# Kernel tuning notes

Hardware: AMD Instinct MI355X
Metric: run time of the kernel (lower is better)

The kernel has to match this reference:

```python
import jax, jax.numpy as jnp
import numpy as np

B, T, INPUT_DIM = 4, 2048, 1024
N_HEADS, HEAD_DIM, EMB_DIM = 16, 64, 1024


def setup_inputs() -> dict:
    key = jax.random.key(0)
    ks = jax.random.split(key, 7)
    s = 0.02
    return {
        "k": jax.random.normal(ks[0], (B, T, INPUT_DIM), jnp.float32),
        "q": jax.random.normal(ks[1], (B, T, INPUT_DIM), jnp.float32),
        "v": jax.random.normal(ks[2], (B, T, INPUT_DIM), jnp.float32),
        # weights stored [in, out] (torch Linear applies x @ W.T with W [out,in])
        "w_key": jax.random.normal(ks[3], (INPUT_DIM, N_HEADS * HEAD_DIM), jnp.float32) * s,
        "w_query": jax.random.normal(ks[4], (INPUT_DIM, N_HEADS * HEAD_DIM), jnp.float32) * s,
        "w_value": jax.random.normal(ks[5], (INPUT_DIM, N_HEADS * HEAD_DIM), jnp.float32) * s,
        "w_proj": jax.random.normal(ks[6], (N_HEADS * HEAD_DIM, EMB_DIM), jnp.float32) * s,
    }


def reference(k, q, v, w_key, w_query, w_value, w_proj):
    temperature = np.sqrt(HEAD_DIM).astype(np.float32)
    # projections -> [B, T, H, D]
    kh = (k @ w_key).reshape(B, T, N_HEADS, HEAD_DIM)
    qh = (q @ w_query).reshape(B, T, N_HEADS, HEAD_DIM)
    vh = (v @ w_value).reshape(B, T, N_HEADS, HEAD_DIM)
    # scaled dot-product attention: scores [B, H, T, T]
    scores = jnp.einsum("bqhd,bkhd->bhqk", qh, kh) / temperature
    attn = jax.nn.softmax(scores, axis=-1)
    out = jnp.einsum("bhqk,bkhd->bqhd", attn, vh).reshape(B, T, N_HEADS * HEAD_DIM)
    return out @ w_proj
```

## Files before the change

### kernel.cpp

```cpp
#include <hip/hip_runtime.h>

typedef unsigned short bf16_t;
typedef __attribute__((ext_vector_type(8))) short short8;
typedef __attribute__((ext_vector_type(4))) float f32x4;
typedef __attribute__((ext_vector_type(16))) float f32x16;
typedef __attribute__((ext_vector_type(4))) unsigned short usx4;

#define T_SEQ 2048
#define NHEAD 16

__device__ __forceinline__ unsigned short f2bf(float x) {
  union { float f; unsigned u; } v; v.f = x;
  unsigned r = v.u + 0x7fffu + ((v.u >> 16) & 1u);
  return (unsigned short)(r >> 16);
}

__device__ __forceinline__ void gld_lds16(const void* g, void* l) {
  __builtin_amdgcn_global_load_lds((const __attribute__((address_space(1))) void*)g,
                                   (__attribute__((address_space(3))) void*)l, 16, 0, 0);
}

__device__ __forceinline__ unsigned cvtpk(float lo, float hi) {
  unsigned r;
  asm("v_cvt_pk_bf16_f32 %0, %1, %2" : "=v"(r) : "v"(lo), "v"(hi));
  return r;
}

__global__ __launch_bounds__(256) void cvt3(const float* __restrict__ a,
                                            const float* __restrict__ b,
                                            const float* __restrict__ c,
                                            bf16_t* __restrict__ oa,
                                            bf16_t* __restrict__ ob,
                                            bf16_t* __restrict__ oc, int n4seg) {
  int i = blockIdx.x * 256 + threadIdx.x;
  const int stride = gridDim.x * 256;
  const int total = 3 * n4seg;
  for (; i < total; i += stride) {
    const int seg = i / n4seg;
    const int j = i - seg * n4seg;
    const float* in = (seg == 0) ? a : (seg == 1) ? b : c;
    bf16_t* out = (seg == 0) ? oa : (seg == 1) ? ob : oc;
    const float4 v = ((const float4*)in)[j];
    usx4 w = { f2bf(v.x), f2bf(v.y), f2bf(v.z), f2bf(v.w) };
    ((usx4*)out)[j] = w;
  }
}

__global__ __launch_bounds__(256) void wtrans(const float* __restrict__ w0, const float* __restrict__ w1,
                                              const float* __restrict__ w2, const float* __restrict__ w3,
                                              bf16_t* __restrict__ wt) {
  __shared__ float tile[32][33];
  const float* w = (blockIdx.z == 0) ? w0 : (blockIdx.z == 1) ? w1 : (blockIdx.z == 2) ? w2 : w3;
  bf16_t* o = wt + (size_t)blockIdx.z * 1024 * 1024;
  const int c = threadIdx.x & 31;
  const int r = threadIdx.x >> 5;
  const int k0 = blockIdx.y * 32, n0 = blockIdx.x * 32;
#pragma unroll
  for (int rr = 0; rr < 32; rr += 8)
    tile[r + rr][c] = w[(size_t)(k0 + r + rr) * 1024 + n0 + c];
  __syncthreads();
#pragma unroll
  for (int rr = 0; rr < 32; rr += 8)
    o[(size_t)(n0 + r + rr) * 1024 + k0 + c] = f2bf(tile[c][r + rr]);
}

__global__ __launch_bounds__(256) void gemm_qkv(const bf16_t* __restrict__ A0,
                                                const bf16_t* __restrict__ A1,
                                                const bf16_t* __restrict__ A2,
                                                const bf16_t* __restrict__ Wt,
                                                bf16_t* __restrict__ C0,
                                                bf16_t* __restrict__ C1,
                                                bf16_t* __restrict__ C2) {
  __shared__ bf16_t As[2][128 * 64];
  __shared__ bf16_t Bs[2][128 * 64];
  const int K = 1024;
  const int z = blockIdx.z;
  const bf16_t* A  = (z == 0) ? A0 : (z == 1) ? A1 : A2;
  const bf16_t* Bt = Wt + (size_t)z * 1024 * 1024;
  const int tid = threadIdx.x;
  const int lane = tid & 63;
  const int l15 = lane & 15;
  const int g = lane >> 4;
  const int wave = tid >> 6;
  const int wr = wave >> 1, wc = wave & 1;
  const int f = blockIdx.x + (int)gridDim.x * blockIdx.y;
  const int fp = (f & 7) * 64 + (f >> 3);
  const int col0 = (fp & 7) * 128, row0 = (fp >> 3) * 128;

  f32x4 acc[4][4];
#pragma unroll
  for (int m = 0; m < 4; ++m)
#pragma unroll
    for (int n = 0; n < 4; ++n) acc[m][n] = (f32x4){0.f, 0.f, 0.f, 0.f};

  const int r_st = tid >> 3;
  const int c_st = tid & 7;

  auto stage = [&](int kt, int bi) {
#pragma unroll
    for (int i = 0; i < 4; ++i) {
      const int r = r_st + i * 32;
      gld_lds16(A  + (size_t)(row0 + r) * K + kt + c_st * 8, As[bi] + (size_t)(tid + i * 256) * 8);
      gld_lds16(Bt + (size_t)(col0 + r) * K + kt + c_st * 8, Bs[bi] + (size_t)(tid + i * 256) * 8);
    }
  };

  const int NIT = K / 64;
  stage(0, 0);
  stage(64, 1);

  for (int it = 0; it < NIT; ++it) {
    const int cur = it & 1;
    if (it + 1 < NIT) { asm volatile("s_waitcnt vmcnt(8)" ::: "memory"); }
    else              { asm volatile("s_waitcnt vmcnt(0)" ::: "memory"); }
    __builtin_amdgcn_s_barrier();
    __builtin_amdgcn_sched_barrier(0);
#pragma unroll
    for (int ks = 0; ks < 2; ++ks) {
      short8 a[4], b[4];
#pragma unroll
      for (int m = 0; m < 4; ++m)
        a[m] = *(const short8*)(As[cur] + (wr * 64 + m * 16 + l15) * 64 + ks * 32 + g * 8);
#pragma unroll
      for (int n = 0; n < 4; ++n)
        b[n] = *(const short8*)(Bs[cur] + (wc * 64 + n * 16 + l15) * 64 + ks * 32 + g * 8);
#pragma unroll
      for (int m = 0; m < 4; ++m)
#pragma unroll
        for (int n = 0; n < 4; ++n)
          acc[m][n] = __builtin_amdgcn_mfma_f32_16x16x32_bf16(a[m], b[n], acc[m][n], 0, 0, 0);
    }
    __builtin_amdgcn_s_barrier();
    __builtin_amdgcn_sched_barrier(0);
    if (it + 2 < NIT) stage((it + 2) * 64, cur);
  }

  if (z == 2) {
#pragma unroll
    for (int m = 0; m < 4; ++m) {
      const int row = row0 + wr * 64 + m * 16 + g * 4;
      const int bb = row >> 11;
      const int t = row & 2047;
#pragma unroll
      for (int n = 0; n < 4; ++n) {
        const int col = col0 + wc * 64 + n * 16 + l15;
        const int hh = col >> 6, dd = col & 63;
        usx4 w = { f2bf(acc[m][n][0]), f2bf(acc[m][n][1]), f2bf(acc[m][n][2]), f2bf(acc[m][n][3]) };
        *(usx4*)(C2 + (((size_t)(bb * 16 + hh) * 64 + dd) * 2048 + t)) = w;
      }
    }
  } else {
    const float sc = (z == 1) ? 0.18033688011112042f : 1.0f;
    bf16_t* C = (z == 1) ? C1 : C0;
#pragma unroll
    for (int m = 0; m < 4; ++m) {
      const int row = row0 + wr * 64 + m * 16 + g * 4;
#pragma unroll
      for (int n = 0; n < 4; ++n) {
        const int col = col0 + wc * 64 + n * 16 + l15;
#pragma unroll
        for (int i = 0; i < 4; ++i)
          C[(size_t)(row + i) * 1024 + col] = f2bf(acc[m][n][i] * sc);
      }
    }
  }
}

__global__ __launch_bounds__(256) void gemm_proj(const bf16_t* __restrict__ A,
                                                 const bf16_t* __restrict__ Bt,
                                                 float* __restrict__ C, int K) {
  __shared__ bf16_t As[2][128 * 64];
  __shared__ bf16_t Bs[2][128 * 64];
  const int tid = threadIdx.x;
  const int lane = tid & 63;
  const int l15 = lane & 15;
  const int g = lane >> 4;
  const int wave = tid >> 6;
  const int wr = wave >> 1, wc = wave & 1;
  const int f = blockIdx.x + (int)gridDim.x * blockIdx.y;
  const int fp = (f & 7) * 64 + (f >> 3);
  const int col0 = (fp & 7) * 128, row0 = (fp >> 3) * 128;

  f32x4 acc[4][4];
#pragma unroll
  for (int m = 0; m < 4; ++m)
#pragma unroll
    for (int n = 0; n < 4; ++n) acc[m][n] = (f32x4){0.f, 0.f, 0.f, 0.f};

  const int r_st = tid >> 3;
  const int c_st = tid & 7;

  auto stage = [&](int kt, int bi) {
#pragma unroll
    for (int i = 0; i < 4; ++i) {
      const int r = r_st + i * 32;
      gld_lds16(A  + (size_t)(row0 + r) * K + kt + c_st * 8, As[bi] + (size_t)(tid + i * 256) * 8);
      gld_lds16(Bt + (size_t)(col0 + r) * K + kt + c_st * 8, Bs[bi] + (size_t)(tid + i * 256) * 8);
    }
  };

  const int NIT = K / 64;
  stage(0, 0);
  stage(64, 1);

  for (int it = 0; it < NIT; ++it) {
    const int cur = it & 1;
    if (it + 1 < NIT) { asm volatile("s_waitcnt vmcnt(8)" ::: "memory"); }
    else              { asm volatile("s_waitcnt vmcnt(0)" ::: "memory"); }
    __builtin_amdgcn_s_barrier();
    __builtin_amdgcn_sched_barrier(0);
#pragma unroll
    for (int ks = 0; ks < 2; ++ks) {
      short8 a[4], b[4];
#pragma unroll
      for (int m = 0; m < 4; ++m)
        a[m] = *(const short8*)(As[cur] + (wr * 64 + m * 16 + l15) * 64 + ks * 32 + g * 8);
#pragma unroll
      for (int n = 0; n < 4; ++n)
        b[n] = *(const short8*)(Bs[cur] + (wc * 64 + n * 16 + l15) * 64 + ks * 32 + g * 8);
#pragma unroll
      for (int m = 0; m < 4; ++m)
#pragma unroll
        for (int n = 0; n < 4; ++n)
          acc[m][n] = __builtin_amdgcn_mfma_f32_16x16x32_bf16(a[m], b[n], acc[m][n], 0, 0, 0);
    }
    __builtin_amdgcn_s_barrier();
    __builtin_amdgcn_sched_barrier(0);
    if (it + 2 < NIT) stage((it + 2) * 64, cur);
  }

#pragma unroll
  for (int m = 0; m < 4; ++m) {
    const int row = row0 + wr * 64 + m * 16 + g * 4;
#pragma unroll
    for (int n = 0; n < 4; ++n) {
      const int col = col0 + wc * 64 + n * 16 + l15;
#pragma unroll
      for (int i = 0; i < 4; ++i)
        C[(size_t)(row + i) * 1024 + col] = acc[m][n][i];
    }
  }
}

__global__ __launch_bounds__(256) void attn_fwd(const bf16_t* __restrict__ qh,
                                                const bf16_t* __restrict__ kh,
                                                const bf16_t* __restrict__ vt,
                                                bf16_t* __restrict__ ao) {
  __shared__ bf16_t smem[24576];
  const int tid = threadIdx.x;
  const int lane = tid & 63;
  const int l31 = lane & 31;
  const int half = lane >> 5;
  const int wave = tid >> 6;
  const int f = blockIdx.x + (int)gridDim.x * blockIdx.y;
  const int fp = (f & 7) * 128 + (f >> 3);
  const int qblk = fp & 15;
  const int bh = fp >> 4;
  const int b = bh >> 4, h = bh & 15;

  const int tq = qblk * 128 + wave * 32 + l31;
  const size_t qoff = (size_t)(b * T_SEQ + tq) * 1024 + h * 64;
  short8 qf[4];
#pragma unroll
  for (int ks = 0; ks < 4; ++ks)
    qf[ks] = *(const short8*)(qh + qoff + ks * 16 + half * 8);

  union { short8 v; unsigned u[4]; } onesf;
#pragma unroll
  for (int i = 0; i < 4; ++i) onesf.u[i] = 0x3F803F80u;

  f32x16 ov0, ov1, lacc, zv;
#pragma unroll
  for (int i = 0; i < 16; ++i) { ov0[i] = 0.f; ov1[i] = 0.f; lacc[i] = 0.f; zv[i] = 0.f; }

  int off[2][4];
#pragma unroll
  for (int k = 0; k < 4; ++k) {
    const int swz = ((k * 2 + half) ^ (l31 & 7)) * 8;
    off[0][k] = l31 * 64 + swz;
    off[1][k] = (32 + l31) * 64 + swz;
  }

  const size_t kbase = (size_t)b * T_SEQ * 1024 + h * 64;
  const size_t vbase = (size_t)bh * 64 * T_SEQ;
  const int r_st = tid >> 3;
  const int cd = tid & 7;

  bf16_t* p0 = smem;
  bf16_t* p1 = smem + 8192;
  bf16_t* p2 = smem + 16384;

  auto stage = [&](int kvt, bf16_t* buf) {
    const int t0 = kvt * 64;
#pragma unroll
    for (int i = 0; i < 2; ++i) {
      const int r = r_st + i * 32;
      const int cs = cd ^ (r & 7);
      gld_lds16(kh + kbase + (size_t)(t0 + r) * 1024 + cs * 8, buf + (size_t)(tid + i * 256) * 8);
      gld_lds16(vt + vbase + (size_t)r * T_SEQ + t0 + cs * 8,  buf + 4096 + (size_t)(tid + i * 256) * 8);
    }
  };

  const int NT = T_SEQ / 64;
  stage(0, p0);
  stage(1, p1);
  asm volatile("s_waitcnt vmcnt(0)" ::: "memory");

  for (int kv = 0; kv < NT; ++kv) {
    if (kv + 1 < NT) { asm volatile("s_waitcnt vmcnt(4)" ::: "memory"); }
    else             { asm volatile("s_waitcnt vmcnt(0)" ::: "memory"); }
    __builtin_amdgcn_s_barrier();
    __builtin_amdgcn_sched_barrier(0);
    if (kv + 2 < NT) stage(kv + 2, p2);

    const bf16_t* Ks = p0;
    const bf16_t* Vs = p0 + 4096;

    f32x16 st[2];
    __builtin_amdgcn_s_setprio(1);
#pragma unroll
    for (int t = 0; t < 2; ++t) {
      const short8 af0 = *(const short8*)(Ks + off[t][0]);
      st[t] = __builtin_amdgcn_mfma_f32_32x32x16_bf16(af0, qf[0], zv, 0, 0, 0);
#pragma unroll
      for (int ks = 1; ks < 4; ++ks) {
        const short8 af = *(const short8*)(Ks + off[t][ks]);
        st[t] = __builtin_amdgcn_mfma_f32_32x32x16_bf16(af, qf[ks], st[t], 0, 0, 0);
      }
    }
    __builtin_amdgcn_s_setprio(0);

#pragma unroll
    for (int t = 0; t < 2; ++t)
#pragma unroll
      for (int i = 0; i < 16; ++i)
        st[t][i] = __builtin_amdgcn_exp2f(st[t][i]);

#pragma unroll
    for (int s = 0; s < 4; ++s) {
      const int t = s >> 1, base = (s & 1) * 8;
      unsigned c0 = cvtpk(st[t][base + 0], st[t][base + 1]);
      unsigned c1 = cvtpk(st[t][base + 2], st[t][base + 3]);
      unsigned c2 = cvtpk(st[t][base + 4], st[t][base + 5]);
      unsigned c3 = cvtpk(st[t][base + 6], st[t][base + 7]);
      asm("v_permlane32_swap_b32 %0, %1" : "+v"(c0), "+v"(c2));
      asm("v_permlane32_swap_b32 %0, %1" : "+v"(c1), "+v"(c3));
      union { short8 v; unsigned u[4]; } bu;
      bu.u[0] = c0; bu.u[1] = c1; bu.u[2] = c2; bu.u[3] = c3;
      __builtin_amdgcn_s_setprio(1);
      lacc = __builtin_amdgcn_mfma_f32_32x32x16_bf16(onesf.v, bu.v, lacc, 0, 0, 0);
      const short8 av0 = *(const short8*)(Vs + off[0][s]);
      ov0 = __builtin_amdgcn_mfma_f32_32x32x16_bf16(av0, bu.v, ov0, 0, 0, 0);
      const short8 av1 = *(const short8*)(Vs + off[1][s]);
      ov1 = __builtin_amdgcn_mfma_f32_32x32x16_bf16(av1, bu.v, ov1, 0, 0, 0);
      __builtin_amdgcn_s_setprio(0);
    }

    bf16_t* tmp = p0; p0 = p1; p1 = p2; p2 = tmp;
  }

  const float inv = 1.f / lacc[0];
  bf16_t* obuf = smem + wave * 2048;
#pragma unroll
  for (int k = 0; k < 4; ++k) {
    usx4 w0 = { f2bf(ov0[4 * k + 0] * inv), f2bf(ov0[4 * k + 1] * inv),
                f2bf(ov0[4 * k + 2] * inv), f2bf(ov0[4 * k + 3] * inv) };
    *(usx4*)(obuf + l31 * 64 + ((k ^ (l31 & 7)) * 8) + half * 4) = w0;
    usx4 w1 = { f2bf(ov1[4 * k + 0] * inv), f2bf(ov1[4 * k + 1] * inv),
                f2bf(ov1[4 * k + 2] * inv), f2bf(ov1[4 * k + 3] * inv) };
    *(usx4*)(obuf + l31 * 64 + (((4 + k) ^ (l31 & 7)) * 8) + half * 4) = w1;
  }
  __syncthreads();
  const int r = lane >> 1;
  const int cb = (lane & 1) * 4;
  const size_t orow = (size_t)(b * T_SEQ + qblk * 128 + wave * 32 + r) * 1024 + h * 64;
#pragma unroll
  for (int c = 0; c < 4; ++c) {
    const int ch = cb + c;
    const short8 v = *(const short8*)(obuf + r * 64 + ((ch ^ (r & 7)) * 8));
    *(short8*)(ao + orow + ch * 8) = v;
  }
}

extern "C" void kernel_launch(void* const* d_in, const int* in_sizes, int n_in,
                              void* d_out, int out_size, void* d_ws, size_t ws_size,
                              hipStream_t stream) {
  const float* k_in  = (const float*)d_in[0];
  const float* q_in  = (const float*)d_in[1];
  const float* v_in  = (const float*)d_in[2];
  const float* w_key = (const float*)d_in[3];
  const float* w_qry = (const float*)d_in[4];
  const float* w_val = (const float*)d_in[5];
  const float* w_prj = (const float*)d_in[6];

  char* ws = (char*)d_ws;
  bf16_t* xb0 = (bf16_t*)(ws);
  bf16_t* xb1 = (bf16_t*)(ws + (16u << 20));
  bf16_t* xb2 = (bf16_t*)(ws + (32u << 20));
  bf16_t* wt  = (bf16_t*)(ws + (48u << 20));
  bf16_t* qh  = (bf16_t*)(ws + (56u << 20));
  bf16_t* kh  = (bf16_t*)(ws + (72u << 20));
  bf16_t* vt  = (bf16_t*)(ws + (88u << 20));
  bf16_t* ao  = (bf16_t*)(ws);

  wtrans<<<dim3(32, 32, 4), 256, 0, stream>>>(w_key, w_qry, w_val, w_prj, wt);

  const int N4 = (8192 * 1024) / 4;
  cvt3<<<3072, 256, 0, stream>>>(k_in, q_in, v_in, xb0, xb1, xb2, N4);

  gemm_qkv<<<dim3(8, 64, 3), 256, 0, stream>>>(xb0, xb1, xb2, wt, kh, qh, vt);

  attn_fwd<<<dim3(16, 64), 256, 0, stream>>>(qh, kh, vt, ao);

  gemm_proj<<<dim3(8, 64), 256, 0, stream>>>(ao, wt + 3u * (1u << 20), (float*)d_out, 1024);
}
```

Before: 226.8 us.

## Split attention into single-wave blocks with private double-buffered K/V tiles

The attention kernel moves from 256-thread blocks, where four waves share 64-key K/V tiles through a triple-buffered LDS ring with block barriers, to 64-thread blocks. Each wave now owns 32 queries, streams 32-key tiles into its own double buffer, and synchronises only through vmcnt waits. V offsets and staging addresses are remapped to the smaller tile shape, and the grid grows four-fold to match. The aim is to remove barrier stalls and let waves run independently, at the cost of losing K/V reuse across waves, which means about four times more K/V loads from L2 and more, smaller loop iterations.

```diff
diff --git a/kernel.cpp b/kernel.cpp
--- a/kernel.cpp
+++ b/kernel.cpp
@@ -242,23 +242,21 @@
   }
 }
 
-__global__ __launch_bounds__(256) void attn_fwd(const bf16_t* __restrict__ qh,
-                                                const bf16_t* __restrict__ kh,
-                                                const bf16_t* __restrict__ vt,
-                                                bf16_t* __restrict__ ao) {
-  __shared__ bf16_t smem[24576];
-  const int tid = threadIdx.x;
-  const int lane = tid & 63;
+__global__ __launch_bounds__(64) void attn_fwd(const bf16_t* __restrict__ qh,
+                                               const bf16_t* __restrict__ kh,
+                                               const bf16_t* __restrict__ vt,
+                                               bf16_t* __restrict__ ao) {
+  __shared__ bf16_t smem[8192];
+  const int lane = threadIdx.x;
   const int l31 = lane & 31;
   const int half = lane >> 5;
-  const int wave = tid >> 6;
   const int f = blockIdx.x + (int)gridDim.x * blockIdx.y;
-  const int fp = (f & 7) * 128 + (f >> 3);
-  const int qblk = fp & 15;
-  const int bh = fp >> 4;
+  const int fp = (f & 7) * 512 + (f >> 3);
+  const int qgrp = fp & 63;
+  const int bh = fp >> 6;
   const int b = bh >> 4, h = bh & 15;
 
-  const int tq = qblk * 128 + wave * 32 + l31;
+  const int tq = qgrp * 32 + l31;
   const size_t qoff = (size_t)(b * T_SEQ + tq) * 1024 + h * 64;
   short8 qf[4];
 #pragma unroll
@@ -273,94 +271,98 @@
 #pragma unroll
   for (int i = 0; i < 16; ++i) { ov0[i] = 0.f; ov1[i] = 0.f; lacc[i] = 0.f; zv[i] = 0.f; }
 
-  int off[2][4];
-#pragma unroll
-  for (int k = 0; k < 4; ++k) {
-    const int swz = ((k * 2 + half) ^ (l31 & 7)) * 8;
-    off[0][k] = l31 * 64 + swz;
-    off[1][k] = (32 + l31) * 64 + swz;
-  }
+  int koff[4];
+#pragma unroll
+  for (int ks = 0; ks < 4; ++ks)
+    koff[ks] = l31 * 64 + (((ks * 2 + half) ^ (l31 & 7)) * 8);
+  int voff[2][2];
+#pragma unroll
+  for (int dt = 0; dt < 2; ++dt)
+#pragma unroll
+    for (int s = 0; s < 2; ++s) {
+      const int r2 = dt * 16 + (l31 >> 1);
+      voff[dt][s] = r2 * 64 + ((((l31 & 1) * 4 + s * 2 + half) ^ (r2 & 7)) * 8);
+    }
 
   const size_t kbase = (size_t)b * T_SEQ * 1024 + h * 64;
   const size_t vbase = (size_t)bh * 64 * T_SEQ;
-  const int r_st = tid >> 3;
-  const int cd = tid & 7;
-
-  bf16_t* p0 = smem;
-  bf16_t* p1 = smem + 8192;
-  bf16_t* p2 = smem + 16384;
-
-  auto stage = [&](int kvt, bf16_t* buf) {
-    const int t0 = kvt * 64;
-#pragma unroll
-    for (int i = 0; i < 2; ++i) {
-      const int r = r_st + i * 32;
-      const int cs = cd ^ (r & 7);
-      gld_lds16(kh + kbase + (size_t)(t0 + r) * 1024 + cs * 8, buf + (size_t)(tid + i * 256) * 8);
-      gld_lds16(vt + vbase + (size_t)r * T_SEQ + t0 + cs * 8,  buf + 4096 + (size_t)(tid + i * 256) * 8);
+  const int r_k = lane >> 3;
+  const int c_k = lane & 7;
+
+  auto stage = [&](int kvt, int bi) {
+    bf16_t* bufK = smem + bi * 4096;
+    bf16_t* bufV = bufK + 2048;
+    const int t0 = kvt * 32;
+#pragma unroll
+    for (int i = 0; i < 4; ++i) {
+      const int r = r_k + i * 8;
+      const int cs = c_k ^ (r & 7);
+      gld_lds16(kh + kbase + (size_t)(t0 + r) * 1024 + cs * 8,
+                bufK + (size_t)(i * 64 + lane) * 8);
+      const int d = r * 2 + (cs >> 2);
+      const int tkc = cs & 3;
+      gld_lds16(vt + vbase + (size_t)d * 2048 + t0 + tkc * 8,
+                bufV + (size_t)(i * 64 + lane) * 8);
     }
   };
 
-  const int NT = T_SEQ / 64;
-  stage(0, p0);
-  stage(1, p1);
+  const int NT = T_SEQ / 32;
+  stage(0, 0);
+  stage(1, 1);
   asm volatile("s_waitcnt vmcnt(0)" ::: "memory");
 
   for (int kv = 0; kv < NT; ++kv) {
-    if (kv + 1 < NT) { asm volatile("s_waitcnt vmcnt(4)" ::: "memory"); }
-    else             { asm volatile("s_waitcnt vmcnt(0)" ::: "memory"); }
-    __builtin_amdgcn_s_barrier();
-    __builtin_amdgcn_sched_barrier(0);
-    if (kv + 2 < NT) stage(kv + 2, p2);
-
-    const bf16_t* Ks = p0;
-    const bf16_t* Vs = p0 + 4096;
-
-    f32x16 st[2];
+    if (kv > 0) {
+      if (kv + 1 < NT) { asm volatile("s_waitcnt vmcnt(8)" ::: "memory"); }
+      else             { asm volatile("s_waitcnt vmcnt(0)" ::: "memory"); }
+    }
+    __builtin_amdgcn_sched_barrier(0);
+    const bf16_t* bufK = smem + (kv & 1) * 4096;
+    const bf16_t* bufV = bufK + 2048;
+
+    f32x16 st;
     __builtin_amdgcn_s_setprio(1);
-#pragma unroll
-    for (int t = 0; t < 2; ++t) {
-      const short8 af0 = *(const short8*)(Ks + off[t][0]);
-      st[t] = __builtin_amdgcn_mfma_f32_32x32x16_bf16(af0, qf[0], zv, 0, 0, 0);
+    {
+      const short8 af0 = *(const short8*)(bufK + koff[0]);
+      st = __builtin_amdgcn_mfma_f32_32x32x16_bf16(af0, qf[0], zv, 0, 0, 0);
 #pragma unroll
       for (int ks = 1; ks < 4; ++ks) {
-        const short8 af = *(const short8*)(Ks + off[t][ks]);
-        st[t] = __builtin_amdgcn_mfma_f32_32x32x16_bf16(af, qf[ks], st[t], 0, 0, 0);
+        const short8 af = *(const short8*)(bufK + koff[ks]);
+        st = __builtin_amdgcn_mfma_f32_32x32x16_bf16(af, qf[ks], st, 0, 0, 0);
       }
     }
     __builtin_amdgcn_s_setprio(0);
 
 #pragma unroll
-    for (int t = 0; t < 2; ++t)
-#pragma unroll
-      for (int i = 0; i < 16; ++i)
-        st[t][i] = __builtin_amdgcn_exp2f(st[t][i]);
-
-#pragma unroll
-    for (int s = 0; s < 4; ++s) {
-      const int t = s >> 1, base = (s & 1) * 8;
-      unsigned c0 = cvtpk(st[t][base + 0], st[t][base + 1]);
-      unsigned c1 = cvtpk(st[t][base + 2], st[t][base + 3]);
-      unsigned c2 = cvtpk(st[t][base + 4], st[t][base + 5]);
-      unsigned c3 = cvtpk(st[t][base + 6], st[t][base + 7]);
+    for (int i = 0; i < 16; ++i)
+      st[i] = __builtin_amdgcn_exp2f(st[i]);
+
+#pragma unroll
+    for (int s = 0; s < 2; ++s) {
+      const int base = s * 8;
+      unsigned c0 = cvtpk(st[base + 0], st[base + 1]);
+      unsigned c1 = cvtpk(st[base + 2], st[base + 3]);
+      unsigned c2 = cvtpk(st[base + 4], st[base + 5]);
+      unsigned c3 = cvtpk(st[base + 6], st[base + 7]);
       asm("v_permlane32_swap_b32 %0, %1" : "+v"(c0), "+v"(c2));
       asm("v_permlane32_swap_b32 %0, %1" : "+v"(c1), "+v"(c3));
       union { short8 v; unsigned u[4]; } bu;
       bu.u[0] = c0; bu.u[1] = c1; bu.u[2] = c2; bu.u[3] = c3;
       __builtin_amdgcn_s_setprio(1);
       lacc = __builtin_amdgcn_mfma_f32_32x32x16_bf16(onesf.v, bu.v, lacc, 0, 0, 0);
-      const short8 av0 = *(const short8*)(Vs + off[0][s]);
+      const short8 av0 = *(const short8*)(bufV + voff[0][s]);
       ov0 = __builtin_amdgcn_mfma_f32_32x32x16_bf16(av0, bu.v, ov0, 0, 0, 0);
-      const short8 av1 = *(const short8*)(Vs + off[1][s]);
+      const short8 av1 = *(const short8*)(bufV + voff[1][s]);
       ov1 = __builtin_amdgcn_mfma_f32_32x32x16_bf16(av1, bu.v, ov1, 0, 0, 0);
       __builtin_amdgcn_s_setprio(0);
     }
 
-    bf16_t* tmp = p0; p0 = p1; p1 = p2; p2 = tmp;
+    __builtin_amdgcn_sched_barrier(0);
+    if (kv + 2 < NT) stage(kv + 2, kv & 1);
   }
 
   const float inv = 1.f / lacc[0];
-  bf16_t* obuf = smem + wave * 2048;
+  bf16_t* obuf = smem;
 #pragma unroll
   for (int k = 0; k < 4; ++k) {
     usx4 w0 = { f2bf(ov0[4 * k + 0] * inv), f2bf(ov0[4 * k + 1] * inv),
@@ -373,7 +375,7 @@
   __syncthreads();
   const int r = lane >> 1;
   const int cb = (lane & 1) * 4;
-  const size_t orow = (size_t)(b * T_SEQ + qblk * 128 + wave * 32 + r) * 1024 + h * 64;
+  const size_t orow = (size_t)(b * T_SEQ + qgrp * 32 + r) * 1024 + h * 64;
 #pragma unroll
   for (int c = 0; c < 4; ++c) {
     const int ch = cb + c;
@@ -410,7 +412,7 @@
 
   gemm_qkv<<<dim3(8, 64, 3), 256, 0, stream>>>(xb0, xb1, xb2, wt, kh, qh, vt);
 
-  attn_fwd<<<dim3(16, 64), 256, 0, stream>>>(qh, kh, vt, ao);
+  attn_fwd<<<dim3(64, 64), 64, 0, stream>>>(qh, kh, vt, ao);
 
   gemm_proj<<<dim3(8, 64), 256, 0, stream>>>(ao, wt + 3u * (1u << 20), (float*)d_out, 1024);
 }
```

New measurement: 273.7 us. +20.7%, slower.
